# Optimization experiments

Hardware: AMD Instinct MI355X
Metric: run time of the kernel (lower is better)

Reference implementation:

```python
import jax, jax.numpy as jnp
import numpy as np

N_IN, C, T, E, N_OUT, F = 50000, 64, 8, 800000, 50000, 64


def setup_inputs() -> dict:
    key = jax.random.key(0)
    k0, k1, k2, k3, k4 = jax.random.split(key, 5)
    node_features = jax.random.normal(k0, (N_IN, C), dtype=jnp.float32)
    edge_features = jax.random.normal(k1, (T, E), dtype=jnp.float32)
    idx_out = jax.random.randint(k2, (E,), 0, N_OUT)
    idx_in = jax.random.randint(k3, (E,), 0, N_IN)
    indices = jnp.stack([idx_out, idx_in], axis=1).astype(jnp.int64)  # [E, 2]
    # glorot-ish scale for kernel [T, C, F]
    scale = np.sqrt(2.0 / (C + F)).astype(np.float32)
    kernel = jax.random.normal(k4, (T, C, F), dtype=jnp.float32) * scale
    bias = jnp.zeros((F,), dtype=jnp.float32)
    return {
        "node_features": node_features,
        "edge_features": edge_features,
        "indices": indices,
        "kernel": kernel,
        "bias": bias,
        "out_size": N_OUT,
    }


def reference(node_features, edge_features, indices, kernel, bias, out_size):
    # sparse_conv (combine='unstack'):
    #   out[i] = sum_t ( segment_sum_{e: out(e)=i} ef[t,e] * x[in(e)] ) @ kernel[t] + bias
    gathered = node_features[indices[:, 1]]          # [E, C] irregular gather
    seg_ids = indices[:, 0]
    n_terms = kernel.shape[0]                        # small fixed structural dim
    out = jnp.zeros((out_size, kernel.shape[2]), dtype=node_features.dtype)
    for t in range(n_terms):
        weighted = edge_features[t][:, None] * gathered            # [E, C]
        agg = jax.ops.segment_sum(weighted, seg_ids, num_segments=out_size)  # [No, C]
        out = out + agg @ kernel[t]                                # [No, F]
    return out + bias
```

## Files before the change

### kernel.cpp

```cpp
#include <hip/hip_runtime.h>

constexpr int N_IN  = 50000;
constexpr int C     = 64;
constexpr int T     = 8;
constexpr int E     = 800000;
constexpr int N_OUT = 50000;
constexpr int F     = 64;

constexpr int CHUNK   = 4096;
constexpr int NCHUNK  = (E + CHUNK - 1) / CHUNK;
constexpr int NBIN_S  = (N_OUT + 255) / 256;
constexpr int LEN_CNT = NBIN_S * NCHUNK;
constexpr int SCA     = (LEN_CNT + 255) / 256;

constexpr size_t OFF_NFBF  = 0;
constexpr size_t OFF_KT    = 6400000;
constexpr size_t OFF_CNT   = OFF_KT + 65536;
constexpr size_t OFF_BSUM  = OFF_CNT + 153664;
constexpr size_t OFF_START = OFF_BSUM + 1024;
constexpr size_t OFF_EFH   = OFF_START + 200064;
constexpr size_t OFF_ENT   = OFF_EFH + 12800000;
constexpr size_t OFF_ENT2  = OFF_ENT + 3200000;
constexpr size_t OFF_BINW  = OFF_ENT2 + 3200000;
static_assert(OFF_EFH % 16 == 0 && OFF_BINW % 16 == 0, "alignment");

typedef __attribute__((ext_vector_type(8))) short short8;
typedef __attribute__((ext_vector_type(4))) float f32x4;
typedef __attribute__((ext_vector_type(8))) _Float16 f16x8;

__device__ inline unsigned short f2bf(float x) {
    unsigned int u = __float_as_uint(x);
    unsigned int r = (u + 0x7FFFu + ((u >> 16) & 1u)) >> 16;
    return (unsigned short)r;
}
__device__ inline float bf2f(unsigned short u) {
    return __uint_as_float(((unsigned int)u) << 16);
}

constexpr int NF_BLOCKS = N_IN * C / 4 / 256;
constexpr int KT_BLOCKS = 32;
constexpr int ET_BLOCKS = E / 256;
constexpr int BH_BLOCKS = NCHUNK;

__global__ __launch_bounds__(256) void prep_kernel(const float* __restrict__ nf,
                                                   const float* __restrict__ Kmat,
                                                   const float* __restrict__ ef,
                                                   const int* __restrict__ idx,
                                                   unsigned short* __restrict__ nf_bf,
                                                   unsigned short* __restrict__ K_T,
                                                   _Float16* __restrict__ efh,
                                                   int* __restrict__ counts) {
    __shared__ int hist[NBIN_S];
    const int b   = blockIdx.x;
    const int tid = threadIdx.x;

    if (b < NF_BLOCKS) {
        int i = b * 256 + tid;
        float4 v = ((const float4*)nf)[i];
        unsigned int u0 = (unsigned int)f2bf(v.x) | ((unsigned int)f2bf(v.y) << 16);
        unsigned int u1 = (unsigned int)f2bf(v.z) | ((unsigned int)f2bf(v.w) << 16);
        ((uint2*)nf_bf)[i] = make_uint2(u0, u1);
    } else if (b < NF_BLOCKS + KT_BLOCKS) {
        for (int k = (b - NF_BLOCKS) * 256 + tid; k < T * C * F; k += KT_BLOCKS * 256) {
            int f = k & 63;
            int c = (k >> 6) & 63;
            int t = k >> 12;
            K_T[f * 512 + t * 64 + c] = f2bf(Kmat[k]);
        }
    } else if (b < NF_BLOCKS + KT_BLOCKS + ET_BLOCKS) {
        int e = (b - NF_BLOCKS - KT_BLOCKS) * 256 + tid;
        f16x8 h;
#pragma unroll
        for (int t = 0; t < T; ++t)
            h[t] = (_Float16)ef[(size_t)t * E + e];
        *(f16x8*)(efh + (size_t)e * 8) = h;
    } else {
        const int c = b - NF_BLOCKS - KT_BLOCKS - ET_BLOCKS;
        for (int i = tid; i < NBIN_S; i += 256) hist[i] = 0;
        __syncthreads();
        const int e0 = c * CHUNK;
        const int n  = min(CHUNK, E - e0);
        for (int i = tid; i < n; i += 256) {
            int o = ((const int2*)idx)[e0 + i].x;
            atomicAdd(&hist[o >> 8], 1);
        }
        __syncthreads();
        for (int i = tid; i < NBIN_S; i += 256)
            counts[i * NCHUNK + c] = hist[i];
    }
}

__global__ __launch_bounds__(256) void scanA_kernel(int* __restrict__ a,
                                                    int* __restrict__ bsum) {
    __shared__ int sh[256];
    const int tid = threadIdx.x;
    int g = blockIdx.x * 256 + tid;
    int v = (g < LEN_CNT) ? a[g] : 0;
    sh[tid] = v;
    __syncthreads();
#pragma unroll
    for (int off = 1; off < 256; off <<= 1) {
        int x = 0;
        if (tid >= off) x = sh[tid - off];
        __syncthreads();
        if (tid >= off) sh[tid] += x;
        __syncthreads();
    }
    int incl = sh[tid];
    if (g < LEN_CNT) a[g] = incl - v;
    if (tid == 255) bsum[blockIdx.x] = incl;
}

__global__ __launch_bounds__(256) void scanBC_kernel(int* __restrict__ a,
                                                     const int* __restrict__ bsum) {
    __shared__ int sh[256];
    const int bi  = blockIdx.x;
    const int tid = threadIdx.x;
    sh[tid] = (tid < bi) ? bsum[tid] : 0;
    __syncthreads();
#pragma unroll
    for (int off = 128; off >= 1; off >>= 1) {
        if (tid < off) sh[tid] += sh[tid + off];
        __syncthreads();
    }
    const int offset = sh[0];
    int g = bi * 256 + tid;
    if (g < LEN_CNT) a[g] += offset;
}

__global__ __launch_bounds__(512) void binscatter_kernel(const int* __restrict__ idx,
                                                         const int* __restrict__ offs,
                                                         const _Float16* __restrict__ efh,
                                                         unsigned* __restrict__ ent,
                                                         _Float16* __restrict__ binw) {
    __shared__ int cur[NBIN_S];
    const int tid = threadIdx.x;
    const int c   = blockIdx.x;
    const f16x8* efh8 = (const f16x8*)efh;
    f16x8* binw8 = (f16x8*)binw;
    for (int i = tid; i < NBIN_S; i += 512) cur[i] = offs[i * NCHUNK + c];
    __syncthreads();
    const int e0 = c * CHUNK;
    const int n  = min(CHUNK, E - e0);
    for (int i = tid; i < n; i += 512) {
        int2 oi = ((const int2*)idx)[e0 + i];
        int bin = oi.x >> 8;
        int loc = oi.x & 255;
        f16x8 w = efh8[e0 + i];
        int pos = atomicAdd(&cur[bin], 1);
        ent[pos]   = ((unsigned)loc << 16) | (unsigned)oi.y;
        binw8[pos] = w;
    }
}

__global__ __launch_bounds__(512) void permfix_kernel(const int* __restrict__ offs,
                                                      const unsigned* __restrict__ ent,
                                                      int* __restrict__ start_g,
                                                      unsigned* __restrict__ ent2) {
    __shared__ int hist[256];
    __shared__ int sc[256];
    __shared__ int cur[256];
    const int tid = threadIdx.x;
    const int b   = blockIdx.x;
    const int W0  = offs[b * NCHUNK];
    const int W1  = (b + 1 < NBIN_S) ? offs[(b + 1) * NCHUNK] : E;

    if (tid < 256) hist[tid] = 0;
    __syncthreads();
    for (int i = W0 + tid; i < W1; i += 512)
        atomicAdd(&hist[ent[i] >> 16], 1);
    __syncthreads();

    if (tid < 256) sc[tid] = hist[tid];
    __syncthreads();
    for (int off = 1; off < 256; off <<= 1) {
        int x = 0;
        if (tid < 256 && tid >= off) x = sc[tid - off];
        __syncthreads();
        if (tid < 256 && tid >= off) sc[tid] += x;
        __syncthreads();
    }
    if (tid < 256) {
        int s = W0 + sc[tid] - hist[tid];
        int g = b * 256 + tid;
        if (g < N_OUT) start_g[g] = s;
        cur[tid] = s;
    }
    if (b == NBIN_S - 1 && tid == 0) start_g[N_OUT] = E;
    __syncthreads();

    for (int i = W0 + tid; i < W1; i += 512) {
        unsigned u = ent[i];
        int loc = (int)(u >> 16);
        int pos = atomicAdd(&cur[loc], 1);
        ent2[pos] = ((unsigned)(i - W0) << 16) | (u & 0xFFFFu);
    }
}

__global__ __launch_bounds__(256) void aggregate_kernel(const unsigned short* __restrict__ nf_bf,
                                                        const unsigned short* __restrict__ K_T,
                                                        const int* __restrict__ start,
                                                        const unsigned* __restrict__ ent2,
                                                        const _Float16* __restrict__ binw,
                                                        const int* __restrict__ offs,
                                                        const float* __restrict__ bias,
                                                        float* __restrict__ out) {
    __shared__ unsigned short A_lds[16][520];

    constexpr int NWG = N_OUT / 16;
    constexpr int Q = NWG / 8, R = NWG % 8;
    const int xc = blockIdx.x & 7;
    const int sl = blockIdx.x >> 3;
    const int orig = (xc < R ? xc * (Q + 1) : R * (Q + 1) + (xc - R) * Q) + sl;

    const int wave = threadIdx.x >> 6;
    const int lane = threadIdx.x & 63;
    const int node_base = orig * 16;
    const int Wbase = offs[(orig >> 4) * NCHUNK];

    const f16x8* binw8 = (const f16x8*)binw;

    for (int q = 0; q < 4; ++q) {
        const int m = wave * 4 + q;
        const int o = node_base + m;
        const int s0 = __builtin_amdgcn_readfirstlane(start[o]);
        const int s1 = __builtin_amdgcn_readfirstlane(start[o + 1]);

        float acc[8] = {0.f, 0.f, 0.f, 0.f, 0.f, 0.f, 0.f, 0.f};

        for (int base = s0; base < s1; base += 64) {
            const int cnt = min(64, s1 - base);
            int vv = (base + lane < s1) ? (int)ent2[base + lane] : 0;

            int j = 0;
            for (; j + 4 <= cnt; j += 4) {
                const int v0 = __builtin_amdgcn_readlane(vv, j + 0);
                const int v1 = __builtin_amdgcn_readlane(vv, j + 1);
                const int v2 = __builtin_amdgcn_readlane(vv, j + 2);
                const int v3 = __builtin_amdgcn_readlane(vv, j + 3);
                float x0 = bf2f(nf_bf[(size_t)(v0 & 0xFFFF) * 64 + lane]);
                float x1 = bf2f(nf_bf[(size_t)(v1 & 0xFFFF) * 64 + lane]);
                float x2 = bf2f(nf_bf[(size_t)(v2 & 0xFFFF) * 64 + lane]);
                float x3 = bf2f(nf_bf[(size_t)(v3 & 0xFFFF) * 64 + lane]);
                f16x8 w0 = binw8[(size_t)(Wbase + (v0 >> 16))];
                f16x8 w1 = binw8[(size_t)(Wbase + (v1 >> 16))];
                f16x8 w2 = binw8[(size_t)(Wbase + (v2 >> 16))];
                f16x8 w3 = binw8[(size_t)(Wbase + (v3 >> 16))];
#pragma unroll
                for (int t = 0; t < T; ++t) {
                    acc[t] += (float)w0[t] * x0;
                    acc[t] += (float)w1[t] * x1;
                    acc[t] += (float)w2[t] * x2;
                    acc[t] += (float)w3[t] * x3;
                }
            }
            for (; j < cnt; ++j) {
                const int v0 = __builtin_amdgcn_readlane(vv, j);
                float x0 = bf2f(nf_bf[(size_t)(v0 & 0xFFFF) * 64 + lane]);
                f16x8 w0 = binw8[(size_t)(Wbase + (v0 >> 16))];
#pragma unroll
                for (int t = 0; t < T; ++t) acc[t] += (float)w0[t] * x0;
            }
        }

#pragma unroll
        for (int t = 0; t < T; ++t) A_lds[m][t * 64 + lane] = f2bf(acc[t]);
    }
    __syncthreads();

    const int mrow = lane & 15;
    const int kb   = lane >> 4;
    const int fcol = wave * 16 + mrow;

    f32x4 acc4 = {0.f, 0.f, 0.f, 0.f};
#pragma unroll
    for (int s = 0; s < 16; ++s) {
        const int k0 = s * 32 + kb * 8;
        short8 a = *(const short8*)&A_lds[mrow][k0];
        short8 b = *(const short8*)(K_T + (size_t)fcol * 512 + k0);
        acc4 = __builtin_amdgcn_mfma_f32_16x16x32_bf16(a, b, acc4, 0, 0, 0);
    }

    const float bv = bias[fcol];
#pragma unroll
    for (int r = 0; r < 4; ++r) {
        const int m = kb * 4 + r;
        out[(size_t)(node_base + m) * F + fcol] = acc4[r] + bv;
    }
}

extern "C" void kernel_launch(void* const* d_in, const int* in_sizes, int n_in,
                              void* d_out, int out_size, void* d_ws, size_t ws_size,
                              hipStream_t stream) {
    const float* nf   = (const float*)d_in[0];
    const float* ef   = (const float*)d_in[1];
    const int*   idx  = (const int*)d_in[2];
    const float* Kmat = (const float*)d_in[3];
    const float* bias = (const float*)d_in[4];
    float*       out  = (float*)d_out;

    char* ws = (char*)d_ws;
    unsigned short* nf_bf  = (unsigned short*)(ws + OFF_NFBF);
    unsigned short* K_T    = (unsigned short*)(ws + OFF_KT);
    int*            counts = (int*)(ws + OFF_CNT);
    int*            bsum   = (int*)(ws + OFF_BSUM);
    int*            start  = (int*)(ws + OFF_START);
    _Float16*       efh    = (_Float16*)(ws + OFF_EFH);
    unsigned*       ent    = (unsigned*)(ws + OFF_ENT);
    unsigned*       ent2   = (unsigned*)(ws + OFF_ENT2);
    _Float16*       binw   = (_Float16*)(ws + OFF_BINW);

    prep_kernel<<<NF_BLOCKS + KT_BLOCKS + ET_BLOCKS + BH_BLOCKS, 256, 0, stream>>>(
        nf, Kmat, ef, idx, nf_bf, K_T, efh, counts);
    scanA_kernel<<<SCA, 256, 0, stream>>>(counts, bsum);
    scanBC_kernel<<<SCA, 256, 0, stream>>>(counts, bsum);
    binscatter_kernel<<<NCHUNK, 512, 0, stream>>>(idx, counts, efh, ent, binw);
    permfix_kernel<<<NBIN_S, 512, 0, stream>>>(counts, ent, start, ent2);
    aggregate_kernel<<<N_OUT / 16, 256, 0, stream>>>(
        nf_bf, K_T, start, ent2, binw, counts, bias, out);
}
```

Measured before the change: 184.1 us.

## Drop fp16 edge-weight pre-pass; scatter fp32 weights directly in binscatter

Removes the separate transpose/convert pass that packed edge features to fp16 in prep_kernel. Binscatter now reads the T strided fp32 rows itself and writes fp32 weights in bin order, which saves one full read+write of the edge-weight array. The aggregate kernel reads fp32 weights, doubling those gather bytes. The chunk size is halved to give binscatter more blocks, the scan handles 512 elements per block to match, and permfix uses 1024 threads.

```diff
diff --git a/kernel.cpp b/kernel.cpp
--- a/kernel.cpp
+++ b/kernel.cpp
@@ -7,26 +7,24 @@
 constexpr int N_OUT = 50000;
 constexpr int F     = 64;
 
-constexpr int CHUNK   = 4096;
+constexpr int CHUNK   = 2048;
 constexpr int NCHUNK  = (E + CHUNK - 1) / CHUNK;
 constexpr int NBIN_S  = (N_OUT + 255) / 256;
 constexpr int LEN_CNT = NBIN_S * NCHUNK;
-constexpr int SCA     = (LEN_CNT + 255) / 256;
+constexpr int SCA     = (LEN_CNT + 511) / 512;
 
 constexpr size_t OFF_NFBF  = 0;
 constexpr size_t OFF_KT    = 6400000;
 constexpr size_t OFF_CNT   = OFF_KT + 65536;
-constexpr size_t OFF_BSUM  = OFF_CNT + 153664;
+constexpr size_t OFF_BSUM  = OFF_CNT + 306544;
 constexpr size_t OFF_START = OFF_BSUM + 1024;
-constexpr size_t OFF_EFH   = OFF_START + 200064;
-constexpr size_t OFF_ENT   = OFF_EFH + 12800000;
+constexpr size_t OFF_ENT   = OFF_START + 200064;
 constexpr size_t OFF_ENT2  = OFF_ENT + 3200000;
 constexpr size_t OFF_BINW  = OFF_ENT2 + 3200000;
-static_assert(OFF_EFH % 16 == 0 && OFF_BINW % 16 == 0, "alignment");
+static_assert(OFF_BINW % 16 == 0 && OFF_ENT % 16 == 0, "alignment");
 
 typedef __attribute__((ext_vector_type(8))) short short8;
 typedef __attribute__((ext_vector_type(4))) float f32x4;
-typedef __attribute__((ext_vector_type(8))) _Float16 f16x8;
 
 __device__ inline unsigned short f2bf(float x) {
     unsigned int u = __float_as_uint(x);
@@ -39,16 +37,13 @@
 
 constexpr int NF_BLOCKS = N_IN * C / 4 / 256;
 constexpr int KT_BLOCKS = 32;
-constexpr int ET_BLOCKS = E / 256;
 constexpr int BH_BLOCKS = NCHUNK;
 
 __global__ __launch_bounds__(256) void prep_kernel(const float* __restrict__ nf,
                                                    const float* __restrict__ Kmat,
-                                                   const float* __restrict__ ef,
                                                    const int* __restrict__ idx,
                                                    unsigned short* __restrict__ nf_bf,
                                                    unsigned short* __restrict__ K_T,
-                                                   _Float16* __restrict__ efh,
                                                    int* __restrict__ counts) {
     __shared__ int hist[NBIN_S];
     const int b   = blockIdx.x;
@@ -67,15 +62,8 @@
             int t = k >> 12;
             K_T[f * 512 + t * 64 + c] = f2bf(Kmat[k]);
         }
-    } else if (b < NF_BLOCKS + KT_BLOCKS + ET_BLOCKS) {
-        int e = (b - NF_BLOCKS - KT_BLOCKS) * 256 + tid;
-        f16x8 h;
-#pragma unroll
-        for (int t = 0; t < T; ++t)
-            h[t] = (_Float16)ef[(size_t)t * E + e];
-        *(f16x8*)(efh + (size_t)e * 8) = h;
     } else {
-        const int c = b - NF_BLOCKS - KT_BLOCKS - ET_BLOCKS;
+        const int c = b - NF_BLOCKS - KT_BLOCKS;
         for (int i = tid; i < NBIN_S; i += 256) hist[i] = 0;
         __syncthreads();
         const int e0 = c * CHUNK;
@@ -92,23 +80,26 @@
 
 __global__ __launch_bounds__(256) void scanA_kernel(int* __restrict__ a,
                                                     int* __restrict__ bsum) {
-    __shared__ int sh[256];
-    const int tid = threadIdx.x;
-    int g = blockIdx.x * 256 + tid;
-    int v = (g < LEN_CNT) ? a[g] : 0;
-    sh[tid] = v;
-    __syncthreads();
-#pragma unroll
-    for (int off = 1; off < 256; off <<= 1) {
-        int x = 0;
-        if (tid >= off) x = sh[tid - off];
-        __syncthreads();
-        if (tid >= off) sh[tid] += x;
-        __syncthreads();
-    }
-    int incl = sh[tid];
-    if (g < LEN_CNT) a[g] = incl - v;
-    if (tid == 255) bsum[blockIdx.x] = incl;
+    __shared__ int sc[512];
+    const int tid = threadIdx.x;
+    const int g0  = blockIdx.x * 512;
+    int v0 = (g0 + tid < LEN_CNT) ? a[g0 + tid] : 0;
+    int v1 = (g0 + 256 + tid < LEN_CNT) ? a[g0 + 256 + tid] : 0;
+    sc[tid] = v0;
+    sc[tid + 256] = v1;
+    __syncthreads();
+    for (int off = 1; off < 512; off <<= 1) {
+        int a0 = sc[tid], a1 = sc[tid + 256];
+        int b0 = (tid >= off) ? sc[tid - off] : 0;
+        int b1 = (tid + 256 >= off) ? sc[tid + 256 - off] : 0;
+        __syncthreads();
+        sc[tid] = a0 + b0;
+        sc[tid + 256] = a1 + b1;
+        __syncthreads();
+    }
+    if (g0 + tid < LEN_CNT) a[g0 + tid] = sc[tid] - v0;
+    if (g0 + 256 + tid < LEN_CNT) a[g0 + 256 + tid] = sc[tid + 256] - v1;
+    if (tid == 255) bsum[blockIdx.x] = sc[511];
 }
 
 __global__ __launch_bounds__(256) void scanBC_kernel(int* __restrict__ a,
@@ -124,20 +115,19 @@
         __syncthreads();
     }
     const int offset = sh[0];
-    int g = bi * 256 + tid;
-    if (g < LEN_CNT) a[g] += offset;
+    const int g0 = bi * 512;
+    if (g0 + tid < LEN_CNT) a[g0 + tid] += offset;
+    if (g0 + 256 + tid < LEN_CNT) a[g0 + 256 + tid] += offset;
 }
 
 __global__ __launch_bounds__(512) void binscatter_kernel(const int* __restrict__ idx,
                                                          const int* __restrict__ offs,
-                                                         const _Float16* __restrict__ efh,
+                                                         const float* __restrict__ ef,
                                                          unsigned* __restrict__ ent,
-                                                         _Float16* __restrict__ binw) {
+                                                         float* __restrict__ binw) {
     __shared__ int cur[NBIN_S];
     const int tid = threadIdx.x;
     const int c   = blockIdx.x;
-    const f16x8* efh8 = (const f16x8*)efh;
-    f16x8* binw8 = (f16x8*)binw;
     for (int i = tid; i < NBIN_S; i += 512) cur[i] = offs[i * NCHUNK + c];
     __syncthreads();
     const int e0 = c * CHUNK;
@@ -146,17 +136,21 @@
         int2 oi = ((const int2*)idx)[e0 + i];
         int bin = oi.x >> 8;
         int loc = oi.x & 255;
-        f16x8 w = efh8[e0 + i];
+        float w[8];
+#pragma unroll
+        for (int t = 0; t < T; ++t) w[t] = ef[(size_t)t * E + e0 + i];
         int pos = atomicAdd(&cur[bin], 1);
-        ent[pos]   = ((unsigned)loc << 16) | (unsigned)oi.y;
-        binw8[pos] = w;
-    }
-}
-
-__global__ __launch_bounds__(512) void permfix_kernel(const int* __restrict__ offs,
-                                                      const unsigned* __restrict__ ent,
-                                                      int* __restrict__ start_g,
-                                                      unsigned* __restrict__ ent2) {
+        ent[pos] = ((unsigned)loc << 16) | (unsigned)oi.y;
+        float4* dst = (float4*)(binw + (size_t)pos * 8);
+        dst[0] = make_float4(w[0], w[1], w[2], w[3]);
+        dst[1] = make_float4(w[4], w[5], w[6], w[7]);
+    }
+}
+
+__global__ __launch_bounds__(1024) void permfix_kernel(const int* __restrict__ offs,
+                                                       const unsigned* __restrict__ ent,
+                                                       int* __restrict__ start_g,
+                                                       unsigned* __restrict__ ent2) {
     __shared__ int hist[256];
     __shared__ int sc[256];
     __shared__ int cur[256];
@@ -167,7 +161,7 @@
 
     if (tid < 256) hist[tid] = 0;
     __syncthreads();
-    for (int i = W0 + tid; i < W1; i += 512)
+    for (int i = W0 + tid; i < W1; i += 1024)
         atomicAdd(&hist[ent[i] >> 16], 1);
     __syncthreads();
 
@@ -189,7 +183,7 @@
     if (b == NBIN_S - 1 && tid == 0) start_g[N_OUT] = E;
     __syncthreads();
 
-    for (int i = W0 + tid; i < W1; i += 512) {
+    for (int i = W0 + tid; i < W1; i += 1024) {
         unsigned u = ent[i];
         int loc = (int)(u >> 16);
         int pos = atomicAdd(&cur[loc], 1);
@@ -201,7 +195,7 @@
                                                         const unsigned short* __restrict__ K_T,
                                                         const int* __restrict__ start,
                                                         const unsigned* __restrict__ ent2,
-                                                        const _Float16* __restrict__ binw,
+                                                        const float* __restrict__ binw,
                                                         const int* __restrict__ offs,
                                                         const float* __restrict__ bias,
                                                         float* __restrict__ out) {
@@ -217,8 +211,6 @@
     const int lane = threadIdx.x & 63;
     const int node_base = orig * 16;
     const int Wbase = offs[(orig >> 4) * NCHUNK];
-
-    const f16x8* binw8 = (const f16x8*)binw;
 
     for (int q = 0; q < 4; ++q) {
         const int m = wave * 4 + q;
@@ -242,24 +234,24 @@
                 float x1 = bf2f(nf_bf[(size_t)(v1 & 0xFFFF) * 64 + lane]);
                 float x2 = bf2f(nf_bf[(size_t)(v2 & 0xFFFF) * 64 + lane]);
                 float x3 = bf2f(nf_bf[(size_t)(v3 & 0xFFFF) * 64 + lane]);
-                f16x8 w0 = binw8[(size_t)(Wbase + (v0 >> 16))];
-                f16x8 w1 = binw8[(size_t)(Wbase + (v1 >> 16))];
-                f16x8 w2 = binw8[(size_t)(Wbase + (v2 >> 16))];
-                f16x8 w3 = binw8[(size_t)(Wbase + (v3 >> 16))];
+                const float* w0 = binw + (size_t)(Wbase + (((unsigned)v0) >> 16)) * 8;
+                const float* w1 = binw + (size_t)(Wbase + (((unsigned)v1) >> 16)) * 8;
+                const float* w2 = binw + (size_t)(Wbase + (((unsigned)v2) >> 16)) * 8;
+                const float* w3 = binw + (size_t)(Wbase + (((unsigned)v3) >> 16)) * 8;
 #pragma unroll
                 for (int t = 0; t < T; ++t) {
-                    acc[t] += (float)w0[t] * x0;
-                    acc[t] += (float)w1[t] * x1;
-                    acc[t] += (float)w2[t] * x2;
-                    acc[t] += (float)w3[t] * x3;
+                    acc[t] += w0[t] * x0;
+                    acc[t] += w1[t] * x1;
+                    acc[t] += w2[t] * x2;
+                    acc[t] += w3[t] * x3;
                 }
             }
             for (; j < cnt; ++j) {
                 const int v0 = __builtin_amdgcn_readlane(vv, j);
                 float x0 = bf2f(nf_bf[(size_t)(v0 & 0xFFFF) * 64 + lane]);
-                f16x8 w0 = binw8[(size_t)(Wbase + (v0 >> 16))];
-#pragma unroll
-                for (int t = 0; t < T; ++t) acc[t] += (float)w0[t] * x0;
+                const float* w0 = binw + (size_t)(Wbase + (((unsigned)v0) >> 16)) * 8;
+#pragma unroll
+                for (int t = 0; t < T; ++t) acc[t] += w0[t] * x0;
             }
         }
 
@@ -305,17 +297,16 @@
     int*            counts = (int*)(ws + OFF_CNT);
     int*            bsum   = (int*)(ws + OFF_BSUM);
     int*            start  = (int*)(ws + OFF_START);
-    _Float16*       efh    = (_Float16*)(ws + OFF_EFH);
     unsigned*       ent    = (unsigned*)(ws + OFF_ENT);
     unsigned*       ent2   = (unsigned*)(ws + OFF_ENT2);
-    _Float16*       binw   = (_Float16*)(ws + OFF_BINW);
-
-    prep_kernel<<<NF_BLOCKS + KT_BLOCKS + ET_BLOCKS + BH_BLOCKS, 256, 0, stream>>>(
-        nf, Kmat, ef, idx, nf_bf, K_T, efh, counts);
+    float*          binw   = (float*)(ws + OFF_BINW);
+
+    prep_kernel<<<NF_BLOCKS + KT_BLOCKS + BH_BLOCKS, 256, 0, stream>>>(
+        nf, Kmat, idx, nf_bf, K_T, counts);
     scanA_kernel<<<SCA, 256, 0, stream>>>(counts, bsum);
     scanBC_kernel<<<SCA, 256, 0, stream>>>(counts, bsum);
-    binscatter_kernel<<<NCHUNK, 512, 0, stream>>>(idx, counts, efh, ent, binw);
-    permfix_kernel<<<NBIN_S, 512, 0, stream>>>(counts, ent, start, ent2);
+    binscatter_kernel<<<NCHUNK, 512, 0, stream>>>(idx, counts, ef, ent, binw);
+    permfix_kernel<<<NBIN_S, 1024, 0, stream>>>(counts, ent, start, ent2);
     aggregate_kernel<<<N_OUT / 16, 256, 0, stream>>>(
         nf_bf, K_T, start, ent2, binw, counts, bias, out);
 }
```

Measured after the change: 185.9 us. About the same (+1.0%).
